# Performance work log

Hardware: AMD Instinct MI355X
Metric: run time of the kernel (lower is better)

The kernel has to match this reference:

```python
import jax, jax.numpy as jnp
import numpy as np

B = 16384
NUM_SCIENTISTS = 100000
NUM_PAPERS = 50000
EMB_DIM = 64
T_SP = 819200   # total implicit (rated) entries, avg 50 per scientist
T_SW = 409600   # total wishlist entries, avg 25 per scientist
GLOBAL_MEAN = 3.82


def setup_inputs() -> dict:
    key = jax.random.key(0)
    ks = jax.random.split(key, 10)
    scientist_ids = jax.random.randint(ks[0], (B,), 0, NUM_SCIENTISTS)
    paper_ids = jax.random.randint(ks[1], (B,), 0, NUM_PAPERS)
    sp_idx = jax.random.randint(ks[2], (T_SP,), 0, NUM_PAPERS)
    sp_seg = jnp.sort(jax.random.randint(ks[3], (T_SP,), 0, B))
    sw_idx = jax.random.randint(ks[4], (T_SW,), 0, NUM_PAPERS)
    sw_seg = jnp.sort(jax.random.randint(ks[5], (T_SW,), 0, B))
    # parameters (init: normal std=0.1 for factor tables, zeros for biases)
    scientist_factors = 0.1 * jax.random.normal(ks[6], (NUM_SCIENTISTS, EMB_DIM), dtype=jnp.float32)
    paper_factors = 0.1 * jax.random.normal(ks[7], (NUM_PAPERS, EMB_DIM), dtype=jnp.float32)
    implicit_factors = 0.1 * jax.random.normal(ks[8], (NUM_PAPERS, EMB_DIM), dtype=jnp.float32)
    implicit_wishlist = 0.1 * jax.random.normal(ks[9], (NUM_PAPERS, EMB_DIM), dtype=jnp.float32)
    scientist_bias = jnp.zeros((NUM_SCIENTISTS,), dtype=jnp.float32)
    paper_bias = jnp.zeros((NUM_PAPERS,), dtype=jnp.float32)
    return {
        "scientist_ids": scientist_ids, "paper_ids": paper_ids,
        "sp_idx": sp_idx, "sp_seg": sp_seg,
        "sw_idx": sw_idx, "sw_seg": sw_seg,
        "scientist_factors": scientist_factors, "paper_factors": paper_factors,
        "scientist_bias": scientist_bias, "paper_bias": paper_bias,
        "implicit_factors": implicit_factors, "implicit_wishlist": implicit_wishlist,
    }


def _pooled(table, idx, seg, num_segments):
    """Gather table rows, segment-sum per batch row, divide by sqrt(count); zero for empty segments."""
    rows = table[idx]                                            # [T, D]
    summed = jax.ops.segment_sum(rows, seg, num_segments=num_segments)  # [B, D]
    counts = jax.ops.segment_sum(jnp.ones_like(idx, dtype=table.dtype), seg,
                                 num_segments=num_segments)      # [B]
    inv = jnp.where(counts > 0, jax.lax.rsqrt(jnp.maximum(counts, 1.0)), 0.0)
    return summed * inv[:, None]


def reference(scientist_ids, paper_ids, sp_idx, sp_seg, sw_idx, sw_seg,
              scientist_factors, paper_factors, scientist_bias, paper_bias,
              implicit_factors, implicit_wishlist):
    s_emb = scientist_factors[scientist_ids]        # [B, D]
    p_emb = paper_factors[paper_ids]                # [B, D]
    s_b = scientist_bias[scientist_ids]             # [B]
    p_b = paper_bias[paper_ids]                     # [B]
    y_u = _pooled(implicit_factors, sp_idx, sp_seg, s_emb.shape[0])
    y_u_wl = _pooled(implicit_wishlist, sw_idx, sw_seg, s_emb.shape[0])
    interaction = jnp.sum((s_emb + y_u + y_u_wl) * p_emb, axis=1)
    return interaction + s_b + p_b + jnp.float32(GLOBAL_MEAN)
```

## Files before the change

kernel.cpp:

```cpp
#include <hip/hip_runtime.h>

#define BATCH 16384
#define EMBD 64
#define GLOBAL_MEAN 3.82f

typedef unsigned short u16;

__device__ __forceinline__ u16 f32_to_bf16_rne(float f) {
    unsigned int u = __float_as_uint(f);
    unsigned int lsb = (u >> 16) & 1u;
    u += 0x7fffu + lsb;
    return (u16)(u >> 16);
}
__device__ __forceinline__ float bf16_to_f32(u16 h) {
    return __uint_as_float(((unsigned int)h) << 16);
}

__global__ __launch_bounds__(256) void seg_bounds_fused(
    const int* __restrict__ sp_seg, int n_sp, int* __restrict__ sp_start,
    const int* __restrict__ sw_seg, int n_sw, int* __restrict__ sw_start,
    float* __restrict__ zrowf)
{
    int gi = blockIdx.x * blockDim.x + threadIdx.x;
    if (gi < EMBD) zrowf[gi] = 0.0f;
    int i = gi;
    const int* seg; int n; int* start;
    if (i < n_sp) { seg = sp_seg; n = n_sp; start = sp_start; }
    else {
        i -= n_sp;
        if (i >= n_sw) return;
        seg = sw_seg; n = n_sw; start = sw_start;
    }
    int s = seg[i];
    int sprev = (i == 0) ? -1 : seg[i - 1];
    for (int r = sprev + 1; r <= s; ++r) start[r] = i;
    if (i == n - 1)
        for (int r = s + 1; r <= BATCH; ++r) start[r] = n;
}

__global__ __launch_bounds__(256) void convert_bf16(
    const float* __restrict__ tf, const float* __restrict__ tw,
    u16* __restrict__ f16, u16* __restrict__ w16,
    int elems_per_table, u16* __restrict__ zrow16)
{
    int tid = blockIdx.x * blockDim.x + threadIdx.x;
    if (tid < EMBD) zrow16[tid] = 0;
    int q = elems_per_table >> 2;
    const float* src; u16* dst; int i = tid;
    if (i < q) { src = tf; dst = f16; }
    else {
        i -= q;
        if (i >= q) return;
        src = tw; dst = w16;
    }
    float4 v = *(const float4*)(src + (size_t)i * 4);
    ushort4 o;
    o.x = f32_to_bf16_rne(v.x);
    o.y = f32_to_bf16_rne(v.y);
    o.z = f32_to_bf16_rne(v.z);
    o.w = f32_to_bf16_rne(v.w);
    *(ushort4*)(dst + (size_t)i * 4) = o;
}

__global__ __launch_bounds__(256, 8) void svdpp_fwd_bf16(
    const int* __restrict__ scientist_ids,
    const int* __restrict__ paper_ids,
    const int* __restrict__ sp_idx, const int* __restrict__ sp_start,
    const int* __restrict__ sw_idx, const int* __restrict__ sw_start,
    const float* __restrict__ s_factors,
    const float* __restrict__ p_factors,
    const float* __restrict__ s_bias,
    const float* __restrict__ p_bias,
    const u16* __restrict__ f16,
    const u16* __restrict__ w16,
    const u16* __restrict__ zrow16,
    float* __restrict__ out)
{
    const int wave = (blockIdx.x * blockDim.x + threadIdx.x) >> 6;
    const int lane = threadIdx.x & 63;
    if (wave >= BATCH) return;
    const int row  = wave;
    const int sub  = lane >> 4;
    const int doff = (lane & 15) * 4;

    const int s0 = __builtin_amdgcn_readfirstlane(sp_start[row]);
    const int e0 = __builtin_amdgcn_readfirstlane(sp_start[row + 1]);
    const int s1 = __builtin_amdgcn_readfirstlane(sw_start[row]);
    const int e1 = __builtin_amdgcn_readfirstlane(sw_start[row + 1]);
    const int n0 = e0 - s0;
    const int n1 = e1 - s1;

    const int sid = __builtin_amdgcn_readfirstlane(scientist_ids[row]);
    const int pid = __builtin_amdgcn_readfirstlane(paper_ids[row]);
    const float4 sf = *(const float4*)(s_factors + (size_t)sid * EMBD + doff);
    const float4 pf = *(const float4*)(p_factors + (size_t)pid * EMBD + doff);
    const float sb = s_bias[sid];
    const float pb = p_bias[pid];

    float4 acc0 = {0.f, 0.f, 0.f, 0.f};
    float4 acc1 = {0.f, 0.f, 0.f, 0.f};

    const int m = n0 > n1 ? n0 : n1;

    for (int c = 0; c < m; c += 64) {
        int r0 = n0 - c;
        if (r0 > 0) {
            int lim0 = r0 < 64 ? r0 : 64;
            int i0 = s0 + c + lane;
            int a0 = i0 < e0 ? i0 : e0 - 1;
            int my0 = sp_idx[a0];
            int jm = (lim0 + 3) >> 2;
            for (int step = 0; step < jm; step += 8) {
                ushort4 v[8];
                #pragma unroll
                for (int u = 0; u < 8; ++u) {
                    int k = sub + 4 * (step + u);
                    int idx = __shfl(my0, k, 64);
                    const u16* base = (k < lim0) ? (f16 + (size_t)idx * EMBD) : zrow16;
                    v[u] = *(const ushort4*)(base + doff);
                }
                #pragma unroll
                for (int u = 0; u < 8; ++u) {
                    acc0.x += bf16_to_f32(v[u].x);
                    acc0.y += bf16_to_f32(v[u].y);
                    acc0.z += bf16_to_f32(v[u].z);
                    acc0.w += bf16_to_f32(v[u].w);
                }
            }
        }
        int r1 = n1 - c;
        if (r1 > 0) {
            int lim1 = r1 < 64 ? r1 : 64;
            int i1 = s1 + c + lane;
            int a1 = i1 < e1 ? i1 : e1 - 1;
            int my1 = sw_idx[a1];
            int jm = (lim1 + 3) >> 2;
            for (int step = 0; step < jm; step += 8) {
                ushort4 v[8];
                #pragma unroll
                for (int u = 0; u < 8; ++u) {
                    int k = sub + 4 * (step + u);
                    int idx = __shfl(my1, k, 64);
                    const u16* base = (k < lim1) ? (w16 + (size_t)idx * EMBD) : zrow16;
                    v[u] = *(const ushort4*)(base + doff);
                }
                #pragma unroll
                for (int u = 0; u < 8; ++u) {
                    acc1.x += bf16_to_f32(v[u].x);
                    acc1.y += bf16_to_f32(v[u].y);
                    acc1.z += bf16_to_f32(v[u].z);
                    acc1.w += bf16_to_f32(v[u].w);
                }
            }
        }
    }

    acc0.x += __shfl_xor(acc0.x, 16, 64); acc0.x += __shfl_xor(acc0.x, 32, 64);
    acc0.y += __shfl_xor(acc0.y, 16, 64); acc0.y += __shfl_xor(acc0.y, 32, 64);
    acc0.z += __shfl_xor(acc0.z, 16, 64); acc0.z += __shfl_xor(acc0.z, 32, 64);
    acc0.w += __shfl_xor(acc0.w, 16, 64); acc0.w += __shfl_xor(acc0.w, 32, 64);
    acc1.x += __shfl_xor(acc1.x, 16, 64); acc1.x += __shfl_xor(acc1.x, 32, 64);
    acc1.y += __shfl_xor(acc1.y, 16, 64); acc1.y += __shfl_xor(acc1.y, 32, 64);
    acc1.z += __shfl_xor(acc1.z, 16, 64); acc1.z += __shfl_xor(acc1.z, 32, 64);
    acc1.w += __shfl_xor(acc1.w, 16, 64); acc1.w += __shfl_xor(acc1.w, 32, 64);

    const float inv0 = n0 > 0 ? rsqrtf((float)n0) : 0.f;
    const float inv1 = n1 > 0 ? rsqrtf((float)n1) : 0.f;

    float v = (sf.x + acc0.x * inv0 + acc1.x * inv1) * pf.x
            + (sf.y + acc0.y * inv0 + acc1.y * inv1) * pf.y
            + (sf.z + acc0.z * inv0 + acc1.z * inv1) * pf.z
            + (sf.w + acc0.w * inv0 + acc1.w * inv1) * pf.w;

    v += __shfl_xor(v, 1, 64);
    v += __shfl_xor(v, 2, 64);
    v += __shfl_xor(v, 4, 64);
    v += __shfl_xor(v, 8, 64);

    if (lane == 0)
        out[row] = v + sb + pb + GLOBAL_MEAN;
}

__global__ __launch_bounds__(256, 8) void svdpp_fwd_f32(
    const int* __restrict__ scientist_ids,
    const int* __restrict__ paper_ids,
    const int* __restrict__ sp_idx, const int* __restrict__ sp_start,
    const int* __restrict__ sw_idx, const int* __restrict__ sw_start,
    const float* __restrict__ s_factors,
    const float* __restrict__ p_factors,
    const float* __restrict__ s_bias,
    const float* __restrict__ p_bias,
    const float* __restrict__ imp_f,
    const float* __restrict__ imp_w,
    const float* __restrict__ zrow,
    float* __restrict__ out)
{
    const int wave = (blockIdx.x * blockDim.x + threadIdx.x) >> 6;
    const int lane = threadIdx.x & 63;
    if (wave >= BATCH) return;
    const int row  = wave;
    const int sub  = lane >> 4;
    const int doff = (lane & 15) * 4;

    const int s0 = __builtin_amdgcn_readfirstlane(sp_start[row]);
    const int e0 = __builtin_amdgcn_readfirstlane(sp_start[row + 1]);
    const int s1 = __builtin_amdgcn_readfirstlane(sw_start[row]);
    const int e1 = __builtin_amdgcn_readfirstlane(sw_start[row + 1]);
    const int n0 = e0 - s0;
    const int n1 = e1 - s1;

    const int sid = __builtin_amdgcn_readfirstlane(scientist_ids[row]);
    const int pid = __builtin_amdgcn_readfirstlane(paper_ids[row]);
    const float4 sf = *(const float4*)(s_factors + (size_t)sid * EMBD + doff);
    const float4 pf = *(const float4*)(p_factors + (size_t)pid * EMBD + doff);
    const float sb = s_bias[sid];
    const float pb = p_bias[pid];

    float4 acc0 = {0.f, 0.f, 0.f, 0.f};
    float4 acc1 = {0.f, 0.f, 0.f, 0.f};
    const int m = n0 > n1 ? n0 : n1;

    for (int c = 0; c < m; c += 64) {
        int r0 = n0 - c;
        if (r0 > 0) {
            int lim0 = r0 < 64 ? r0 : 64;
            int i0 = s0 + c + lane;
            int a0 = i0 < e0 ? i0 : e0 - 1;
            int my0 = sp_idx[a0];
            int jm = (lim0 + 3) >> 2;
            for (int step = 0; step < jm; step += 8) {
                float4 v[8];
                #pragma unroll
                for (int u = 0; u < 8; ++u) {
                    int k = sub + 4 * (step + u);
                    int idx = __shfl(my0, k, 64);
                    const float* base = (k < lim0) ? (imp_f + (size_t)idx * EMBD) : zrow;
                    v[u] = *(const float4*)(base + doff);
                }
                #pragma unroll
                for (int u = 0; u < 8; ++u) {
                    acc0.x += v[u].x; acc0.y += v[u].y;
                    acc0.z += v[u].z; acc0.w += v[u].w;
                }
            }
        }
        int r1 = n1 - c;
        if (r1 > 0) {
            int lim1 = r1 < 64 ? r1 : 64;
            int i1 = s1 + c + lane;
            int a1 = i1 < e1 ? i1 : e1 - 1;
            int my1 = sw_idx[a1];
            int jm = (lim1 + 3) >> 2;
            for (int step = 0; step < jm; step += 8) {
                float4 v[8];
                #pragma unroll
                for (int u = 0; u < 8; ++u) {
                    int k = sub + 4 * (step + u);
                    int idx = __shfl(my1, k, 64);
                    const float* base = (k < lim1) ? (imp_w + (size_t)idx * EMBD) : zrow;
                    v[u] = *(const float4*)(base + doff);
                }
                #pragma unroll
                for (int u = 0; u < 8; ++u) {
                    acc1.x += v[u].x; acc1.y += v[u].y;
                    acc1.z += v[u].z; acc1.w += v[u].w;
                }
            }
        }
    }

    acc0.x += __shfl_xor(acc0.x, 16, 64); acc0.x += __shfl_xor(acc0.x, 32, 64);
    acc0.y += __shfl_xor(acc0.y, 16, 64); acc0.y += __shfl_xor(acc0.y, 32, 64);
    acc0.z += __shfl_xor(acc0.z, 16, 64); acc0.z += __shfl_xor(acc0.z, 32, 64);
    acc0.w += __shfl_xor(acc0.w, 16, 64); acc0.w += __shfl_xor(acc0.w, 32, 64);
    acc1.x += __shfl_xor(acc1.x, 16, 64); acc1.x += __shfl_xor(acc1.x, 32, 64);
    acc1.y += __shfl_xor(acc1.y, 16, 64); acc1.y += __shfl_xor(acc1.y, 32, 64);
    acc1.z += __shfl_xor(acc1.z, 16, 64); acc1.z += __shfl_xor(acc1.z, 32, 64);
    acc1.w += __shfl_xor(acc1.w, 16, 64); acc1.w += __shfl_xor(acc1.w, 32, 64);

    const float inv0 = n0 > 0 ? rsqrtf((float)n0) : 0.f;
    const float inv1 = n1 > 0 ? rsqrtf((float)n1) : 0.f;

    float v = (sf.x + acc0.x * inv0 + acc1.x * inv1) * pf.x
            + (sf.y + acc0.y * inv0 + acc1.y * inv1) * pf.y
            + (sf.z + acc0.z * inv0 + acc1.z * inv1) * pf.z
            + (sf.w + acc0.w * inv0 + acc1.w * inv1) * pf.w;

    v += __shfl_xor(v, 1, 64);
    v += __shfl_xor(v, 2, 64);
    v += __shfl_xor(v, 4, 64);
    v += __shfl_xor(v, 8, 64);

    if (lane == 0)
        out[row] = v + sb + pb + GLOBAL_MEAN;
}

extern "C" void kernel_launch(void* const* d_in, const int* in_sizes, int n_in,
                              void* d_out, int out_size, void* d_ws, size_t ws_size,
                              hipStream_t stream) {
    const int* scientist_ids = (const int*)d_in[0];
    const int* paper_ids     = (const int*)d_in[1];
    const int* sp_idx        = (const int*)d_in[2];
    const int* sp_seg        = (const int*)d_in[3];
    const int* sw_idx        = (const int*)d_in[4];
    const int* sw_seg        = (const int*)d_in[5];
    const float* s_factors   = (const float*)d_in[6];
    const float* p_factors   = (const float*)d_in[7];
    const float* s_bias      = (const float*)d_in[8];
    const float* p_bias      = (const float*)d_in[9];
    const float* imp_f       = (const float*)d_in[10];
    const float* imp_w       = (const float*)d_in[11];
    float* out = (float*)d_out;

    const int t_sp = in_sizes[2];
    const int t_sw = in_sizes[4];
    const int tbl_elems = in_sizes[10];

    char* ws = (char*)d_ws;
    float* zrowf  = (float*)ws;
    u16*   zrow16 = (u16*)(ws + 256);
    int* sp_start = (int*)(ws + 512);
    int* sw_start = sp_start + (BATCH + 1);
    size_t off = 512 + (size_t)2 * (BATCH + 1) * 4;
    off = (off + 255) & ~(size_t)255;
    u16* f16 = (u16*)(ws + off);
    u16* w16 = f16 + (size_t)tbl_elems;
    size_t need = off + (size_t)2 * tbl_elems * 2;

    seg_bounds_fused<<<(t_sp + t_sw + 255) / 256, 256, 0, stream>>>(
        sp_seg, t_sp, sp_start, sw_seg, t_sw, sw_start, zrowf);

    const int blocks = (BATCH * 64) / 256;

    if (ws_size >= need) {
        const int cthreads = (tbl_elems >> 2) * 2;
        convert_bf16<<<(cthreads + 255) / 256, 256, 0, stream>>>(
            imp_f, imp_w, f16, w16, tbl_elems, zrow16);
        svdpp_fwd_bf16<<<blocks, 256, 0, stream>>>(
            scientist_ids, paper_ids,
            sp_idx, sp_start, sw_idx, sw_start,
            s_factors, p_factors, s_bias, p_bias,
            f16, w16, zrow16, out);
    } else {
        svdpp_fwd_f32<<<blocks, 256, 0, stream>>>(
            scientist_ids, paper_ids,
            sp_idx, sp_start, sw_idx, sw_start,
            s_factors, p_factors, s_bias, p_bias,
            imp_f, imp_w, zrowf, out);
    }
}
```

Before: 39.04 us.

## Fuse prep kernels and widen bf16 gather loads to 16 bytes per lane

The segment-bounds and bf16 table-conversion kernels are merged into one launch, removing a kernel launch and its boundary. The main kernel now has each lane load 8 bf16 values (uint4) instead of 4, with 8 rows in flight per wave and the inner step loop dropped, so each 64-entry chunk takes a single unrolled batch of 8 loads. The bf16 unpack uses shift and mask directly, the factor and bias loads move after the gather loop, and the occupancy hint drops from 8 to 6. More accumulators per lane raise register pressure, and a wider reduction tree is needed.

```diff
diff --git a/kernel.cpp b/kernel.cpp
--- a/kernel.cpp
+++ b/kernel.cpp
@@ -5,25 +5,40 @@
 #define GLOBAL_MEAN 3.82f
 
 typedef unsigned short u16;
+typedef unsigned int u32;
 
 __device__ __forceinline__ u16 f32_to_bf16_rne(float f) {
-    unsigned int u = __float_as_uint(f);
-    unsigned int lsb = (u >> 16) & 1u;
+    u32 u = __float_as_uint(f);
+    u32 lsb = (u >> 16) & 1u;
     u += 0x7fffu + lsb;
     return (u16)(u >> 16);
 }
-__device__ __forceinline__ float bf16_to_f32(u16 h) {
-    return __uint_as_float(((unsigned int)h) << 16);
-}
-
-__global__ __launch_bounds__(256) void seg_bounds_fused(
+
+__global__ __launch_bounds__(256) void prep_fused(
     const int* __restrict__ sp_seg, int n_sp, int* __restrict__ sp_start,
     const int* __restrict__ sw_seg, int n_sw, int* __restrict__ sw_start,
-    float* __restrict__ zrowf)
+    const float* __restrict__ tf, const float* __restrict__ tw,
+    u16* __restrict__ f16, u16* __restrict__ w16, int tbl_elems,
+    float* __restrict__ zrowf, u16* __restrict__ zrow16)
 {
     int gi = blockIdx.x * blockDim.x + threadIdx.x;
-    if (gi < EMBD) zrowf[gi] = 0.0f;
-    int i = gi;
+    if (gi < EMBD) { zrowf[gi] = 0.0f; zrow16[gi] = 0; }
+
+    const int q = tbl_elems >> 2;
+    if (gi < 2 * q) {
+        const float* src = gi < q ? tf : tw;
+        u16* dst         = gi < q ? f16 : w16;
+        int i            = gi < q ? gi : gi - q;
+        float4 v = *(const float4*)(src + (size_t)i * 4);
+        ushort4 o;
+        o.x = f32_to_bf16_rne(v.x);
+        o.y = f32_to_bf16_rne(v.y);
+        o.z = f32_to_bf16_rne(v.z);
+        o.w = f32_to_bf16_rne(v.w);
+        *(ushort4*)(dst + (size_t)i * 4) = o;
+        return;
+    }
+    int i = gi - 2 * q;
     const int* seg; int n; int* start;
     if (i < n_sp) { seg = sp_seg; n = n_sp; start = sp_start; }
     else {
@@ -38,31 +53,7 @@
         for (int r = s + 1; r <= BATCH; ++r) start[r] = n;
 }
 
-__global__ __launch_bounds__(256) void convert_bf16(
-    const float* __restrict__ tf, const float* __restrict__ tw,
-    u16* __restrict__ f16, u16* __restrict__ w16,
-    int elems_per_table, u16* __restrict__ zrow16)
-{
-    int tid = blockIdx.x * blockDim.x + threadIdx.x;
-    if (tid < EMBD) zrow16[tid] = 0;
-    int q = elems_per_table >> 2;
-    const float* src; u16* dst; int i = tid;
-    if (i < q) { src = tf; dst = f16; }
-    else {
-        i -= q;
-        if (i >= q) return;
-        src = tw; dst = w16;
-    }
-    float4 v = *(const float4*)(src + (size_t)i * 4);
-    ushort4 o;
-    o.x = f32_to_bf16_rne(v.x);
-    o.y = f32_to_bf16_rne(v.y);
-    o.z = f32_to_bf16_rne(v.z);
-    o.w = f32_to_bf16_rne(v.w);
-    *(ushort4*)(dst + (size_t)i * 4) = o;
-}
-
-__global__ __launch_bounds__(256, 8) void svdpp_fwd_bf16(
+__global__ __launch_bounds__(256, 6) void svdpp_fwd_bf16(
     const int* __restrict__ scientist_ids,
     const int* __restrict__ paper_ids,
     const int* __restrict__ sp_idx, const int* __restrict__ sp_start,
@@ -80,8 +71,8 @@
     const int lane = threadIdx.x & 63;
     if (wave >= BATCH) return;
     const int row  = wave;
-    const int sub  = lane >> 4;
-    const int doff = (lane & 15) * 4;
+    const int sub  = lane >> 3;
+    const int doff = (lane & 7) * 8;
 
     const int s0 = __builtin_amdgcn_readfirstlane(sp_start[row]);
     const int e0 = __builtin_amdgcn_readfirstlane(sp_start[row + 1]);
@@ -89,18 +80,25 @@
     const int e1 = __builtin_amdgcn_readfirstlane(sw_start[row + 1]);
     const int n0 = e0 - s0;
     const int n1 = e1 - s1;
-
     const int sid = __builtin_amdgcn_readfirstlane(scientist_ids[row]);
     const int pid = __builtin_amdgcn_readfirstlane(paper_ids[row]);
-    const float4 sf = *(const float4*)(s_factors + (size_t)sid * EMBD + doff);
-    const float4 pf = *(const float4*)(p_factors + (size_t)pid * EMBD + doff);
-    const float sb = s_bias[sid];
-    const float pb = p_bias[pid];
-
-    float4 acc0 = {0.f, 0.f, 0.f, 0.f};
-    float4 acc1 = {0.f, 0.f, 0.f, 0.f};
+
+    float acc0[8] = {0.f,0.f,0.f,0.f,0.f,0.f,0.f,0.f};
+    float acc1[8] = {0.f,0.f,0.f,0.f,0.f,0.f,0.f,0.f};
 
     const int m = n0 > n1 ? n0 : n1;
+
+    #define CVT_ACC(ACC, VV)                                            \
+        do {                                                            \
+            ACC[0] += __uint_as_float((VV).x << 16);                    \
+            ACC[1] += __uint_as_float((VV).x & 0xffff0000u);            \
+            ACC[2] += __uint_as_float((VV).y << 16);                    \
+            ACC[3] += __uint_as_float((VV).y & 0xffff0000u);            \
+            ACC[4] += __uint_as_float((VV).z << 16);                    \
+            ACC[5] += __uint_as_float((VV).z & 0xffff0000u);            \
+            ACC[6] += __uint_as_float((VV).w << 16);                    \
+            ACC[7] += __uint_as_float((VV).w & 0xffff0000u);            \
+        } while (0)
 
     for (int c = 0; c < m; c += 64) {
         int r0 = n0 - c;
@@ -109,24 +107,16 @@
             int i0 = s0 + c + lane;
             int a0 = i0 < e0 ? i0 : e0 - 1;
             int my0 = sp_idx[a0];
-            int jm = (lim0 + 3) >> 2;
-            for (int step = 0; step < jm; step += 8) {
-                ushort4 v[8];
-                #pragma unroll
-                for (int u = 0; u < 8; ++u) {
-                    int k = sub + 4 * (step + u);
-                    int idx = __shfl(my0, k, 64);
-                    const u16* base = (k < lim0) ? (f16 + (size_t)idx * EMBD) : zrow16;
-                    v[u] = *(const ushort4*)(base + doff);
-                }
-                #pragma unroll
-                for (int u = 0; u < 8; ++u) {
-                    acc0.x += bf16_to_f32(v[u].x);
-                    acc0.y += bf16_to_f32(v[u].y);
-                    acc0.z += bf16_to_f32(v[u].z);
-                    acc0.w += bf16_to_f32(v[u].w);
-                }
+            uint4 v[8];
+            #pragma unroll
+            for (int u = 0; u < 8; ++u) {
+                int k = sub + 8 * u;
+                int idx = __shfl(my0, k, 64);
+                const u16* base = (k < lim0) ? (f16 + (size_t)idx * EMBD) : zrow16;
+                v[u] = *(const uint4*)(base + doff);
             }
+            #pragma unroll
+            for (int u = 0; u < 8; ++u) CVT_ACC(acc0, v[u]);
         }
         int r1 = n1 - c;
         if (r1 > 0) {
@@ -134,48 +124,52 @@
             int i1 = s1 + c + lane;
             int a1 = i1 < e1 ? i1 : e1 - 1;
             int my1 = sw_idx[a1];
-            int jm = (lim1 + 3) >> 2;
-            for (int step = 0; step < jm; step += 8) {
-                ushort4 v[8];
-                #pragma unroll
-                for (int u = 0; u < 8; ++u) {
-                    int k = sub + 4 * (step + u);
-                    int idx = __shfl(my1, k, 64);
-                    const u16* base = (k < lim1) ? (w16 + (size_t)idx * EMBD) : zrow16;
-                    v[u] = *(const ushort4*)(base + doff);
-                }
-                #pragma unroll
-                for (int u = 0; u < 8; ++u) {
-                    acc1.x += bf16_to_f32(v[u].x);
-                    acc1.y += bf16_to_f32(v[u].y);
-                    acc1.z += bf16_to_f32(v[u].z);
-                    acc1.w += bf16_to_f32(v[u].w);
-                }
+            uint4 v[8];
+            #pragma unroll
+            for (int u = 0; u < 8; ++u) {
+                int k = sub + 8 * u;
+                int idx = __shfl(my1, k, 64);
+                const u16* base = (k < lim1) ? (w16 + (size_t)idx * EMBD) : zrow16;
+                v[u] = *(const uint4*)(base + doff);
             }
+            #pragma unroll
+            for (int u = 0; u < 8; ++u) CVT_ACC(acc1, v[u]);
         }
     }
-
-    acc0.x += __shfl_xor(acc0.x, 16, 64); acc0.x += __shfl_xor(acc0.x, 32, 64);
-    acc0.y += __shfl_xor(acc0.y, 16, 64); acc0.y += __shfl_xor(acc0.y, 32, 64);
-    acc0.z += __shfl_xor(acc0.z, 16, 64); acc0.z += __shfl_xor(acc0.z, 32, 64);
-    acc0.w += __shfl_xor(acc0.w, 16, 64); acc0.w += __shfl_xor(acc0.w, 32, 64);
-    acc1.x += __shfl_xor(acc1.x, 16, 64); acc1.x += __shfl_xor(acc1.x, 32, 64);
-    acc1.y += __shfl_xor(acc1.y, 16, 64); acc1.y += __shfl_xor(acc1.y, 32, 64);
-    acc1.z += __shfl_xor(acc1.z, 16, 64); acc1.z += __shfl_xor(acc1.z, 32, 64);
-    acc1.w += __shfl_xor(acc1.w, 16, 64); acc1.w += __shfl_xor(acc1.w, 32, 64);
+    #undef CVT_ACC
+
+    #pragma unroll
+    for (int d = 0; d < 8; ++d) {
+        acc0[d] += __shfl_xor(acc0[d], 8, 64);
+        acc0[d] += __shfl_xor(acc0[d], 16, 64);
+        acc0[d] += __shfl_xor(acc0[d], 32, 64);
+        acc1[d] += __shfl_xor(acc1[d], 8, 64);
+        acc1[d] += __shfl_xor(acc1[d], 16, 64);
+        acc1[d] += __shfl_xor(acc1[d], 32, 64);
+    }
 
     const float inv0 = n0 > 0 ? rsqrtf((float)n0) : 0.f;
     const float inv1 = n1 > 0 ? rsqrtf((float)n1) : 0.f;
 
-    float v = (sf.x + acc0.x * inv0 + acc1.x * inv1) * pf.x
-            + (sf.y + acc0.y * inv0 + acc1.y * inv1) * pf.y
-            + (sf.z + acc0.z * inv0 + acc1.z * inv1) * pf.z
-            + (sf.w + acc0.w * inv0 + acc1.w * inv1) * pf.w;
+    const float4 sfa = *(const float4*)(s_factors + (size_t)sid * EMBD + doff);
+    const float4 sfb = *(const float4*)(s_factors + (size_t)sid * EMBD + doff + 4);
+    const float4 pfa = *(const float4*)(p_factors + (size_t)pid * EMBD + doff);
+    const float4 pfb = *(const float4*)(p_factors + (size_t)pid * EMBD + doff + 4);
+    const float sb = s_bias[sid];
+    const float pb = p_bias[pid];
+
+    float v = (sfa.x + acc0[0] * inv0 + acc1[0] * inv1) * pfa.x
+            + (sfa.y + acc0[1] * inv0 + acc1[1] * inv1) * pfa.y
+            + (sfa.z + acc0[2] * inv0 + acc1[2] * inv1) * pfa.z
+            + (sfa.w + acc0[3] * inv0 + acc1[3] * inv1) * pfa.w
+            + (sfb.x + acc0[4] * inv0 + acc1[4] * inv1) * pfb.x
+            + (sfb.y + acc0[5] * inv0 + acc1[5] * inv1) * pfb.y
+            + (sfb.z + acc0[6] * inv0 + acc1[6] * inv1) * pfb.z
+            + (sfb.w + acc0[7] * inv0 + acc1[7] * inv1) * pfb.w;
 
     v += __shfl_xor(v, 1, 64);
     v += __shfl_xor(v, 2, 64);
     v += __shfl_xor(v, 4, 64);
-    v += __shfl_xor(v, 8, 64);
 
     if (lane == 0)
         out[row] = v + sb + pb + GLOBAL_MEAN;
@@ -289,6 +283,7 @@
     v += __shfl_xor(v, 1, 64);
     v += __shfl_xor(v, 2, 64);
     v += __shfl_xor(v, 4, 64);
+
     v += __shfl_xor(v, 8, 64);
 
     if (lane == 0)
@@ -327,21 +322,23 @@
     u16* w16 = f16 + (size_t)tbl_elems;
     size_t need = off + (size_t)2 * tbl_elems * 2;
 
-    seg_bounds_fused<<<(t_sp + t_sw + 255) / 256, 256, 0, stream>>>(
-        sp_seg, t_sp, sp_start, sw_seg, t_sw, sw_start, zrowf);
-
     const int blocks = (BATCH * 64) / 256;
 
     if (ws_size >= need) {
-        const int cthreads = (tbl_elems >> 2) * 2;
-        convert_bf16<<<(cthreads + 255) / 256, 256, 0, stream>>>(
-            imp_f, imp_w, f16, w16, tbl_elems, zrow16);
+        const int q = tbl_elems >> 2;
+        const int prep_threads = 2 * q + t_sp + t_sw;
+        prep_fused<<<(prep_threads + 255) / 256, 256, 0, stream>>>(
+            sp_seg, t_sp, sp_start, sw_seg, t_sw, sw_start,
+            imp_f, imp_w, f16, w16, tbl_elems, zrowf, zrow16);
         svdpp_fwd_bf16<<<blocks, 256, 0, stream>>>(
             scientist_ids, paper_ids,
             sp_idx, sp_start, sw_idx, sw_start,
             s_factors, p_factors, s_bias, p_bias,
             f16, w16, zrow16, out);
     } else {
+        prep_fused<<<(t_sp + t_sw + 255) / 256, 256, 0, stream>>>(
+            sp_seg, t_sp, sp_start, sw_seg, t_sw, sw_start,
+            imp_f, imp_w, (u16*)zrow16, (u16*)zrow16, 0, zrowf, zrow16);
         svdpp_fwd_f32<<<blocks, 256, 0, stream>>>(
             scientist_ids, paper_ids,
             sp_idx, sp_start, sw_idx, sw_start,
```

Result: slower. 83.70 us (+114.4%).
